# Kernel optimization log

Hardware: AMD Instinct MI355X
Metric: run time of the kernel (lower is better)

The kernel has to match this reference:

```python
import jax, jax.numpy as jnp
import numpy as np

EPS_BN = 1e-5


def _square_distance(a, b):
    # a: [B,N,3], b: [B,S,3] -> [B,N,S]
    return (jnp.sum(a * a, -1)[:, :, None]
            - 2.0 * jnp.einsum('bnc,bsc->bns', a, b)
            + jnp.sum(b * b, -1)[:, None, :])


def _bn_relu(x, gamma, beta):
    # x: [B,C,N]; training-mode batch norm over (B,N) per channel
    mean = jnp.mean(x, axis=(0, 2), keepdims=True)
    var = jnp.var(x, axis=(0, 2), keepdims=True)
    y = (x - mean) * jax.lax.rsqrt(var + EPS_BN)
    y = y * gamma[None, :, None] + beta[None, :, None]
    return jax.nn.relu(y)


def setup_inputs() -> dict:
    key = jax.random.key(0)
    ks = jax.random.split(key, 8)
    B, N, S, D1, D2 = 16, 4096, 1024, 128, 256
    Cin, C0, C1 = D1 + D2, 256, 128
    inp = {
        'xyz1': jax.random.normal(ks[0], (B, 3, N), jnp.float32),
        'xyz2': jax.random.normal(ks[1], (B, 3, S), jnp.float32),
        'points1': jax.random.normal(ks[2], (B, D1, N), jnp.float32),
        'points2': jax.random.normal(ks[3], (B, D2, S), jnp.float32),
        # pointwise Conv1d weights (kernel size 1) as [out,in]
        'w0': jax.random.normal(ks[4], (C0, Cin), jnp.float32) * (1.0 / np.sqrt(Cin)),
        'b0': jnp.zeros((C0,), jnp.float32),
        'g0': jnp.ones((C0,), jnp.float32),
        'be0': jnp.zeros((C0,), jnp.float32),
        'w1': jax.random.normal(ks[5], (C1, C0), jnp.float32) * (1.0 / np.sqrt(C0)),
        'b1': jnp.zeros((C1,), jnp.float32),
        'g1': jnp.ones((C1,), jnp.float32),
        'be1': jnp.zeros((C1,), jnp.float32),
    }
    return inp


def reference(xyz1, xyz2, points1, points2, w0, b0, g0, be0, w1, b1, g1, be1):
    # permute to [B,N,3] / [B,S,3] / [B,S,D2]
    x1 = jnp.transpose(xyz1, (0, 2, 1))
    x2 = jnp.transpose(xyz2, (0, 2, 1))
    p2 = jnp.transpose(points2, (0, 2, 1))
    B, N, _ = x1.shape

    dists = _square_distance(x1, x2)            # [B,N,S]
    # NOTE: faithful to the source: idx comes from the sort, but the
    # weight distances are the FIRST 3 columns of the UNsorted dists
    # (the repo assigns sorted values to `dicts`, not `dists`).
    idx = jnp.argsort(dists, axis=-1)[:, :, :3]  # [B,N,3]
    d3 = jnp.maximum(dists[:, :, :3], 1e-10)     # [B,N,3]
    weight = 1.0 / d3
    weight = weight / jnp.sum(weight, axis=-1, keepdims=True)

    gathered = jax.vmap(lambda p, i: p[i])(p2, idx)          # [B,N,3,D2]
    interpolated = jnp.sum(gathered * weight[..., None], axis=2)  # [B,N,D2]

    p1 = jnp.transpose(points1, (0, 2, 1))       # [B,N,D1]
    new_points = jnp.concatenate([p1, interpolated], axis=-1)  # [B,N,Cin]
    new_points = jnp.transpose(new_points, (0, 2, 1))           # [B,Cin,N]

    h = jnp.einsum('oc,bcn->bon', w0, new_points) + b0[None, :, None]
    h = _bn_relu(h, g0, be0)
    h = jnp.einsum('oc,bcn->bon', w1, h) + b1[None, :, None]
    h = _bn_relu(h, g1, be1)
    return h
```

## Files before the change

### kernel.cpp

```cpp
#include <hip/hip_runtime.h>
#include <cstdint>
#include <cstddef>

#define BB   16
#define NN   4096
#define SS   1024
#define D1   128
#define D2   256
#define CIN  384
#define C0   256
#define C1   128
#define MM   (BB*NN)
#define NBLK (MM/128)

typedef __attribute__((ext_vector_type(8))) short short8;
typedef __attribute__((ext_vector_type(4))) float f32x4;

__device__ __forceinline__ float b2f(unsigned short h) {
    union { unsigned int u; float f; } x; x.u = ((unsigned int)h) << 16; return x.f;
}
__device__ __forceinline__ unsigned short f2b(float f) {
    union { float f; unsigned int u; } x; x.f = f;
    unsigned int r = x.u + 0x7FFFu + ((x.u >> 16) & 1u);
    return (unsigned short)(r >> 16);
}

#define GLD16(g, l) __builtin_amdgcn_global_load_lds( \
    (const __attribute__((address_space(1))) void*)(g), \
    (__attribute__((address_space(3))) void*)(l), 16, 0, 0)

__device__ __forceinline__ void knn_body3(const float* __restrict__ xyz1,
                                          const float* __restrict__ xyz2,
                                          int* __restrict__ idxb, float* __restrict__ wtb,
                                          int rb, int t, char* smem)
{
    double* mrg = (double*)smem;
    const int b    = rb >> 6;
    const int lane = t & 63;
    const int n    = (rb & 63) * 64 + lane;
    const int wu   = __builtin_amdgcn_readfirstlane(t >> 6);

    const float* qx = xyz2 + ((size_t)b * 3 + 0) * SS + wu * 256;
    const float* qy = xyz2 + ((size_t)b * 3 + 1) * SS + wu * 256;
    const float* qz = xyz2 + ((size_t)b * 3 + 2) * SS + wu * 256;

    const float px = xyz1[((size_t)b * 3 + 0) * NN + n];
    const float py = xyz1[((size_t)b * 3 + 1) * NN + n];
    const float pz = xyz1[((size_t)b * 3 + 2) * NN + n];

    const double INITK = __hiloint2double(0x7F7FFFFF, 0);
    double A0 = INITK, A1 = INITK, A2 = INITK;
    double B0 = INITK, B1 = INITK, B2 = INITK;
    const int sb = wu * 256;

#pragma unroll 4
    for (int s = 0; s < 256; s += 2) {
        {
            float qxv = qx[s], qyv = qy[s], qzv = qz[s];
            float dx = px - qxv, dy = py - qyv, dz = pz - qzv;
            float d = dx*dx + dy*dy + dz*dz;
            double k = __hiloint2double(__float_as_int(d), sb + s);
            double t0 = fmin(k, A0), h0 = fmax(k, A0);
            double t1 = fmin(h0, A1), h1 = fmax(h0, A1);
            A2 = fmin(h1, A2); A0 = t0; A1 = t1;
        }
        {
            float qxv = qx[s+1], qyv = qy[s+1], qzv = qz[s+1];
            float dx = px - qxv, dy = py - qyv, dz = pz - qzv;
            float d = dx*dx + dy*dy + dz*dz;
            double k = __hiloint2double(__float_as_int(d), sb + s + 1);
            double t0 = fmin(k, B0), h0 = fmax(k, B0);
            double t1 = fmin(h0, B1), h1 = fmax(h0, B1);
            B2 = fmin(h1, B2); B0 = t0; B1 = t1;
        }
    }
    double K0, K1, K2;
    {
        double y0 = fmax(A0, B0);
        K0 = fmin(A0, B0);
        double x1 = fmin(A1, B1);
        K1 = fmin(y0, x1);
        double z  = fmax(y0, x1);
        double x2 = fmin(A2, B2);
        K2 = fmin(z, x2);
    }
    if (wu > 0) {
        mrg[(wu * 64 + lane) * 3 + 0] = K0;
        mrg[(wu * 64 + lane) * 3 + 1] = K1;
        mrg[(wu * 64 + lane) * 3 + 2] = K2;
    }
    __syncthreads();
    if (wu == 0) {
#pragma unroll
        for (int q = 1; q < 4; ++q) {
            double C0d = mrg[(q * 64 + lane) * 3 + 0];
            double C1d = mrg[(q * 64 + lane) * 3 + 1];
            double C2d = mrg[(q * 64 + lane) * 3 + 2];
            double y0 = fmax(K0, C0d);
            K0 = fmin(K0, C0d);
            double x1 = fmin(K1, C1d);
            double nK1 = fmin(y0, x1);
            double z  = fmax(y0, x1);
            double x2 = fmin(K2, C2d);
            K2 = fmin(z, x2);
            K1 = nK1;
        }
        int j0 = __double2loint(K0), j1 = __double2loint(K1), j2 = __double2loint(K2);
        float dd0, dd1, dd2;
        { float dx=px-qx[0], dy=py-qy[0], dz=pz-qz[0]; dd0 = fmaxf(dx*dx+dy*dy+dz*dz, 1e-10f); }
        { float dx=px-qx[1], dy=py-qy[1], dz=pz-qz[1]; dd1 = fmaxf(dx*dx+dy*dy+dz*dz, 1e-10f); }
        { float dx=px-qx[2], dy=py-qy[2], dz=pz-qz[2]; dd2 = fmaxf(dx*dx+dy*dy+dz*dz, 1e-10f); }
        float r0 = 1.f/dd0, r1 = 1.f/dd1, r2 = 1.f/dd2;
        float inv = 1.f / (r0 + r1 + r2);
        size_t base = ((size_t)b * NN + n) * 3;
        idxb[base+0] = j0; idxb[base+1] = j1; idxb[base+2] = j2;
        wtb[base+0] = r0*inv; wtb[base+1] = r1*inv; wtb[base+2] = r2*inv;
    }
}

__device__ __forceinline__ void transpose_body(const float* __restrict__ src,
                                               unsigned short* __restrict__ dst,
                                               int C, int Np, int dstStride,
                                               int b, int cblk, int nblk, int t, char* smem)
{
    float (*tile)[65] = (float(*)[65])smem;
    const int c0 = cblk * 64, n0 = nblk * 64;
    const int j = t & 63, i4 = t >> 6;
#pragma unroll
    for (int p = 0; p < 64; p += 4) {
        int ci = p + i4;
        tile[ci][j] = src[((size_t)b * C + c0 + ci) * Np + n0 + j];
    }
    __syncthreads();
#pragma unroll
    for (int p = 0; p < 64; p += 4) {
        int ni = p + i4;
        dst[((size_t)b * Np + n0 + ni) * dstStride + c0 + j] = f2b(tile[j][ni]);
    }
}

__global__ __launch_bounds__(256) void mega_front_k(
    const float* __restrict__ xyz1, const float* __restrict__ xyz2,
    const float* __restrict__ points1, const float* __restrict__ points2,
    const float* __restrict__ w0, const float* __restrict__ w1,
    unsigned short* __restrict__ P1T, unsigned short* __restrict__ P2T,
    unsigned short* __restrict__ w0b, unsigned short* __restrict__ w1b,
    int* __restrict__ idxb, float* __restrict__ wtb)
{
    __shared__ __align__(16) char smem[16640];
    const unsigned bid = blockIdx.x;
    const int g = bid / 70, r = bid % 70;
    const int t = threadIdx.x;

    if (r < 16) {
        knn_body3(xyz1, xyz2, idxb, wtb, g * 16 + r, t, smem);
    } else if (r < 48) {
        int rb = g * 32 + (r - 16);
        transpose_body(points1, P1T, D1, NN, D1,
                       rb >> 7, (rb >> 6) & 1, rb & 63, t, smem);
    } else if (r < 64) {
        int rb = g * 16 + (r - 48);
        transpose_body(points2, P2T, D2, SS, D2,
                       rb >> 6, (rb >> 4) & 3, rb & 15, t, smem);
    } else {
        int rb = g * 6 + (r - 64);
        int i = rb * 256 + t;
        if (i < C0 * CIN) w0b[i] = f2b(w0[i]);
        if (i < C1 * C0)  w1b[i] = f2b(w1[i]);
    }
}

__launch_bounds__(512, 1)
__global__ void gemm1_k(const unsigned short* __restrict__ P1T,
                        const unsigned short* __restrict__ P2T,
                        const int* __restrict__ idxb, const float* __restrict__ wtb,
                        const unsigned short* __restrict__ w0b,
                        unsigned short* __restrict__ h1, float* __restrict__ part1)
{
    __shared__ unsigned short Als[128 * 64];
    __shared__ unsigned short Bls[256 * 64];
    __shared__ float lsum[2][256];
    __shared__ float lsq[2][256];

    const int t = threadIdx.x;
    const int wv = t >> 6, l = t & 63, g = l >> 4, lc = l & 15;
    const int wm = wv >> 2, wn = wv & 3;
    const int m0 = blockIdx.x * 128;
    const int b  = blockIdx.x >> 5;
    const int sub = t & 7;

    const int grow = t >> 2;
    const size_t gb = ((size_t)(m0 + grow)) * 3;
    const int gi0 = idxb[gb], gi1 = idxb[gb+1], gi2 = idxb[gb+2];
    const float gw0 = wtb[gb], gw1 = wtb[gb+1], gw2 = wtb[gb+2];
    const char* gp0 = (const char*)(P2T + ((size_t)b * SS + gi0) * D2) + (t & 3) * 32;
    const char* gp1 = (const char*)(P2T + ((size_t)b * SS + gi1) * D2) + (t & 3) * 32;
    const char* gp2 = (const char*)(P2T + ((size_t)b * SS + gi2) * D2) + (t & 3) * 32;
    char* gdst = (char*)Als + grow * 128;
    const int gsw = (grow & 7) << 4;

    f32x4 acc[4][4];
#pragma unroll
    for (int i = 0; i < 4; ++i)
#pragma unroll
        for (int j = 0; j < 4; ++j) acc[i][j] = (f32x4){0.f, 0.f, 0.f, 0.f};

    for (int ks = 0; ks < 6; ++ks) {
        const int k0 = ks * 64;
        __syncthreads();
        if (ks < 2) {
#pragma unroll
            for (int q = 0; q < 2; ++q) {
                int row = q * 64 + (t >> 3);
                int bco = (sub * 16) ^ ((row & 7) << 4);
                const char* src = (const char*)P1T + (((size_t)(m0 + row)) * D1 + k0) * 2 + bco;
                char* dst = (char*)Als + (q * 512 + wv * 64) * 16;
                GLD16(src, dst);
            }
        } else {
            const int cgB = (ks - 2) * 128;
#pragma unroll
            for (int h = 0; h < 2; ++h) {
                union { uint4 v; unsigned short s[8]; } a0, a1, a2, ov;
                a0.v = *(const uint4*)(gp0 + cgB + h * 16);
                a1.v = *(const uint4*)(gp1 + cgB + h * 16);
                a2.v = *(const uint4*)(gp2 + cgB + h * 16);
#pragma unroll
                for (int i = 0; i < 8; ++i)
                    ov.s[i] = f2b(gw0 * b2f(a0.s[i]) + gw1 * b2f(a1.s[i]) + gw2 * b2f(a2.s[i]));
                *(uint4*)(gdst + (((t & 3) * 32 + h * 16) ^ gsw)) = ov.v;
            }
        }
#pragma unroll
        for (int q = 0; q < 4; ++q) {
            int o = q * 64 + (t >> 3);
            int bco = (sub * 16) ^ ((o & 7) << 4);
            const char* src = (const char*)w0b + (((size_t)o) * CIN + k0) * 2 + bco;
            char* dst = (char*)Bls + (q * 512 + wv * 64) * 16;
            GLD16(src, dst);
        }
        __syncthreads();
#pragma unroll
        for (int kk = 0; kk < 2; ++kk) {
            short8 af[4], bfr[4];
#pragma unroll
            for (int fm = 0; fm < 4; ++fm) {
                int row = wm * 64 + fm * 16 + lc;
                int bcol = kk * 64 + g * 16;
                af[fm] = *(const short8*)((const char*)Als + row * 128 + (bcol ^ ((row & 7) << 4)));
            }
#pragma unroll
            for (int fn = 0; fn < 4; ++fn) {
                int o = wn * 64 + fn * 16 + lc;
                int bcol = kk * 64 + g * 16;
                bfr[fn] = *(const short8*)((const char*)Bls + o * 128 + (bcol ^ ((o & 7) << 4)));
            }
#pragma unroll
            for (int fm = 0; fm < 4; ++fm)
#pragma unroll
                for (int fn = 0; fn < 4; ++fn)
                    acc[fm][fn] = __builtin_amdgcn_mfma_f32_16x16x32_bf16(af[fm], bfr[fn], acc[fm][fn], 0, 0, 0);
        }
    }

    float s1[4] = {0,0,0,0}, s2v[4] = {0,0,0,0};
#pragma unroll
    for (int fm = 0; fm < 4; ++fm)
#pragma unroll
        for (int fn = 0; fn < 4; ++fn) {
            int row = m0 + wm * 64 + fm * 16 + g * 4;
            int col = wn * 64 + fn * 16 + lc;
#pragma unroll
            for (int j = 0; j < 4; ++j) {
                float v = acc[fm][fn][j];
                h1[((size_t)(row + j)) * C0 + col] = f2b(v);
                s1[fn] += v; s2v[fn] += v * v;
            }
        }
#pragma unroll
    for (int fn = 0; fn < 4; ++fn) {
        s1[fn] += __shfl_xor(s1[fn], 16); s1[fn] += __shfl_xor(s1[fn], 32);
        s2v[fn] += __shfl_xor(s2v[fn], 16); s2v[fn] += __shfl_xor(s2v[fn], 32);
    }
    if (l < 16) {
#pragma unroll
        for (int fn = 0; fn < 4; ++fn) {
            lsum[wm][wn * 64 + fn * 16 + l] = s1[fn];
            lsq[wm][wn * 64 + fn * 16 + l] = s2v[fn];
        }
    }
    __syncthreads();
    if (t < 256) {
        part1[(size_t)t * NBLK + blockIdx.x]        = lsum[0][t] + lsum[1][t];
        part1[(size_t)(C0 + t) * NBLK + blockIdx.x] = lsq[0][t] + lsq[1][t];
    }
}

__global__ void stats_k(const float* __restrict__ part, int nblk, int C,
                        const float* __restrict__ gam, const float* __restrict__ bet,
                        float* __restrict__ sc, float* __restrict__ sh)
{
    const int w = threadIdx.x >> 6, l = threadIdx.x & 63;
    const int o = blockIdx.x * 4 + w;
    if (o >= C) return;
    float s = 0.f, q = 0.f;
    for (int i = l; i < nblk; i += 64) {
        s += part[(size_t)o * nblk + i];
        q += part[(size_t)(C + o) * nblk + i];
    }
#pragma unroll
    for (int r = 32; r; r >>= 1) { s += __shfl_xor(s, r); q += __shfl_xor(q, r); }
    if (l == 0) {
        const float inv = 1.0f / (float)MM;
        float mean = s * inv;
        float var = q * inv - mean * mean;
        float scale = gam[o] * rsqrtf(var + 1e-5f);
        sc[o] = scale;
        sh[o] = bet[o] - mean * scale;
    }
}

__launch_bounds__(256, 1)
__global__ void gemm2_k(const unsigned short* __restrict__ h1, const unsigned short* __restrict__ w1b,
                        const float* __restrict__ sc1, const float* __restrict__ sh1,
                        unsigned short* __restrict__ h2, float* __restrict__ part2)
{
    __shared__ unsigned short Als[128 * 64];
    __shared__ unsigned short Bls[128 * 64];
    __shared__ float scl[256], shl[256];
    __shared__ float lsum[2][128];
    __shared__ float lsq[2][128];

    const int t = threadIdx.x;
    const int wv = t >> 6, l = t & 63, g = l >> 4, lc = l & 15;
    const int wm = wv >> 1, wn = wv & 1;
    const int m0 = blockIdx.x * 128;
    const int sub = t & 7;

    scl[t] = sc1[t]; shl[t] = sh1[t];

    f32x4 acc[4][4];
#pragma unroll
    for (int i = 0; i < 4; ++i)
#pragma unroll
        for (int j = 0; j < 4; ++j) acc[i][j] = (f32x4){0.f, 0.f, 0.f, 0.f};

    for (int ks = 0; ks < 4; ++ks) {
        const int k0 = ks * 64;
        __syncthreads();
        uint4 r[4];
#pragma unroll
        for (int q = 0; q < 4; ++q) {
            int row = q * 32 + (t >> 3);
            r[q] = *(const uint4*)((const char*)h1 + (((size_t)(m0 + row)) * C0 + k0) * 2 + sub * 16);
        }
#pragma unroll
        for (int q = 0; q < 4; ++q) {
            int row = q * 32 + (t >> 3);
            union { uint4 v; unsigned short s[8]; } u, ov;
            u.v = r[q];
#pragma unroll
            for (int i = 0; i < 8; ++i) {
                int k = k0 + sub * 8 + i;
                float f = b2f(u.s[i]);
                ov.s[i] = f2b(fmaxf(0.0f, fmaf(scl[k], f, shl[k])));
            }
            *(uint4*)((char*)Als + row * 128 + ((sub * 16) ^ ((row & 7) << 4))) = ov.v;
        }
#pragma unroll
        for (int q = 0; q < 4; ++q) {
            int o = q * 32 + (t >> 3);
            int bco = (sub * 16) ^ ((o & 7) << 4);
            const char* src = (const char*)w1b + (((size_t)o) * C0 + k0) * 2 + bco;
            char* dst = (char*)Bls + (q * 256 + wv * 64) * 16;
            GLD16(src, dst);
        }
        __syncthreads();
#pragma unroll
        for (int kk = 0; kk < 2; ++kk) {
            short8 af[4], bfr[4];
#pragma unroll
            for (int fm = 0; fm < 4; ++fm) {
                int row = wm * 64 + fm * 16 + lc;
                int bcol = kk * 64 + g * 16;
                af[fm] = *(const short8*)((const char*)Als + row * 128 + (bcol ^ ((row & 7) << 4)));
            }
#pragma unroll
            for (int fn = 0; fn < 4; ++fn) {
                int o = wn * 64 + fn * 16 + lc;
                int bcol = kk * 64 + g * 16;
                bfr[fn] = *(const short8*)((const char*)Bls + o * 128 + (bcol ^ ((o & 7) << 4)));
            }
#pragma unroll
            for (int fm = 0; fm < 4; ++fm)
#pragma unroll
                for (int fn = 0; fn < 4; ++fn)
                    acc[fm][fn] = __builtin_amdgcn_mfma_f32_16x16x32_bf16(af[fm], bfr[fn], acc[fm][fn], 0, 0, 0);
        }
    }

    float s1[4] = {0,0,0,0}, s2v[4] = {0,0,0,0};
#pragma unroll
    for (int fm = 0; fm < 4; ++fm)
#pragma unroll
        for (int fn = 0; fn < 4; ++fn) {
            int row = m0 + wm * 64 + fm * 16 + g * 4;
            int col = wn * 64 + fn * 16 + lc;
#pragma unroll
            for (int j = 0; j < 4; ++j) {
                float v = acc[fm][fn][j];
                h2[((size_t)(row + j)) * C1 + col] = f2b(v);
                s1[fn] += v; s2v[fn] += v * v;
            }
        }
#pragma unroll
    for (int fn = 0; fn < 4; ++fn) {
        s1[fn] += __shfl_xor(s1[fn], 16); s1[fn] += __shfl_xor(s1[fn], 32);
        s2v[fn] += __shfl_xor(s2v[fn], 16); s2v[fn] += __shfl_xor(s2v[fn], 32);
    }
    if (l < 16) {
#pragma unroll
        for (int fn = 0; fn < 4; ++fn) {
            lsum[wm][wn * 64 + fn * 16 + l] = s1[fn];
            lsq[wm][wn * 64 + fn * 16 + l] = s2v[fn];
        }
    }
    __syncthreads();
    if (t < 128) {
        part2[(size_t)t * NBLK + blockIdx.x]        = lsum[0][t] + lsum[1][t];
        part2[(size_t)(C1 + t) * NBLK + blockIdx.x] = lsq[0][t] + lsq[1][t];
    }
}

__global__ void finalize_k(const unsigned short* __restrict__ h2,
                           const float* __restrict__ sc, const float* __restrict__ sh,
                           float* __restrict__ out)
{
    __shared__ float tile[64][65];
    const int b = blockIdx.z, o0 = blockIdx.y * 64, n0 = blockIdx.x * 64;
    const int t = threadIdx.x, j = t & 63, i4 = t >> 6;
    const float scv = sc[o0 + j], shv = sh[o0 + j];
#pragma unroll
    for (int p = 0; p < 64; p += 4) {
        int ni = p + i4;
        float f = b2f(h2[((size_t)b * NN + n0 + ni) * C1 + o0 + j]);
        tile[ni][j] = fmaxf(0.0f, fmaf(scv, f, shv));
    }
    __syncthreads();
#pragma unroll
    for (int p = 0; p < 64; p += 4) {
        int oi = p + i4;
        out[((size_t)(b * C1 + o0 + oi)) * NN + n0 + j] = tile[j][oi];
    }
}

extern "C" void kernel_launch(void* const* d_in, const int* in_sizes, int n_in,
                              void* d_out, int out_size, void* d_ws, size_t ws_size,
                              hipStream_t stream)
{
    const float* xyz1    = (const float*)d_in[0];
    const float* xyz2    = (const float*)d_in[1];
    const float* points1 = (const float*)d_in[2];
    const float* points2 = (const float*)d_in[3];
    const float* w0      = (const float*)d_in[4];
    const float* g0      = (const float*)d_in[6];
    const float* be0     = (const float*)d_in[7];
    const float* w1      = (const float*)d_in[8];
    const float* g1      = (const float*)d_in[10];
    const float* be1     = (const float*)d_in[11];
    float* out = (float*)d_out;
    char* ws = (char*)d_ws;

    unsigned short* P1T = (unsigned short*)(ws + 0);
    unsigned short* h1  = (unsigned short*)(ws + 16777216);
    unsigned short* P2T = (unsigned short*)(ws + 50331648);
    unsigned short* h2  = (unsigned short*)(ws + 58720256);
    int*   idxb  = (int*)  (ws + 75497472);
    float* wtb   = (float*)(ws + 76283904);
    unsigned short* w0b = (unsigned short*)(ws + 77070336);
    unsigned short* w1b = (unsigned short*)(ws + 77266944);
    float* part1 = (float*)(ws + 77332480);
    float* part2 = (float*)(ws + 78381056);
    float* sc1   = (float*)(ws + 78905344);
    float* sh1   = (float*)(ws + 78906368);
    float* sc2   = (float*)(ws + 78907392);
    float* sh2   = (float*)(ws + 78908416);

    mega_front_k<<<70 * 64, 256, 0, stream>>>(xyz1, xyz2, points1, points2, w0, w1,
                                              P1T, P2T, w0b, w1b, idxb, wtb);
    gemm1_k<<<MM/128, 512, 0, stream>>>(P1T, P2T, idxb, wtb, w0b, h1, part1);
    stats_k<<<C0/4, 256, 0, stream>>>(part1, NBLK, C0, g0, be0, sc1, sh1);
    gemm2_k<<<MM/128, 256, 0, stream>>>(h1, w1b, sc1, sh1, h2, part2);
    stats_k<<<C1/4, 256, 0, stream>>>(part2, NBLK, C1, g1, be1, sc2, sh2);
    finalize_k<<<dim3(NN/64, C1/64, BB), 256, 0, stream>>>(h2, sc2, sh2, out);
}
```

Before: 117.3 us.

## Split KNN candidates across 8 lanes with LDS-staged xyz2 and shuffle merge

Restructures the 3-NN search so each block handles 32 query points, with 8 lanes per point each scanning a 128-candidate chunk. Candidate coordinates are first staged into LDS as padded float4 rows, and the per-lane top-3 lists are merged with xor shuffles instead of an LDS merge plus a single-wave tail. This removes repeated global loads of xyz2 and the idle waves during the merge, at the cost of twice as many knn blocks, each with a staging pass and a barrier.

```diff
diff --git a/kernel.cpp b/kernel.cpp
--- a/kernel.cpp
+++ b/kernel.cpp
@@ -29,20 +29,24 @@
     (const __attribute__((address_space(1))) void*)(g), \
     (__attribute__((address_space(3))) void*)(l), 16, 0, 0)
 
-__device__ __forceinline__ void knn_body3(const float* __restrict__ xyz1,
+__device__ __forceinline__ void knn_body5(const float* __restrict__ xyz1,
                                           const float* __restrict__ xyz2,
                                           int* __restrict__ idxb, float* __restrict__ wtb,
                                           int rb, int t, char* smem)
 {
-    double* mrg = (double*)smem;
-    const int b    = rb >> 6;
-    const int lane = t & 63;
-    const int n    = (rb & 63) * 64 + lane;
-    const int wu   = __builtin_amdgcn_readfirstlane(t >> 6);
-
-    const float* qx = xyz2 + ((size_t)b * 3 + 0) * SS + wu * 256;
-    const float* qy = xyz2 + ((size_t)b * 3 + 1) * SS + wu * 256;
-    const float* qz = xyz2 + ((size_t)b * 3 + 2) * SS + wu * 256;
+    float4* cnd = (float4*)smem;
+    const int b    = rb >> 7;
+    const int bx   = rb & 127;
+    const int chunk = t & 7;
+    const int n    = bx * 32 + (t >> 3);
+
+    for (int i = t; i < SS; i += 256) {
+        float qx = xyz2[((size_t)b * 3 + 0) * SS + i];
+        float qy = xyz2[((size_t)b * 3 + 1) * SS + i];
+        float qz = xyz2[((size_t)b * 3 + 2) * SS + i];
+        cnd[(i >> 7) * 129 + (i & 127)] = make_float4(qx, qy, qz, 0.f);
+    }
+    __syncthreads();
 
     const float px = xyz1[((size_t)b * 3 + 0) * NN + n];
     const float py = xyz1[((size_t)b * 3 + 1) * NN + n];
@@ -51,29 +55,31 @@
     const double INITK = __hiloint2double(0x7F7FFFFF, 0);
     double A0 = INITK, A1 = INITK, A2 = INITK;
     double B0 = INITK, B1 = INITK, B2 = INITK;
-    const int sb = wu * 256;
+    const float4* cc = cnd + chunk * 129;
+    const int sbase = chunk * 128;
 
 #pragma unroll 4
-    for (int s = 0; s < 256; s += 2) {
+    for (int c = 0; c < 128; c += 2) {
         {
-            float qxv = qx[s], qyv = qy[s], qzv = qz[s];
-            float dx = px - qxv, dy = py - qyv, dz = pz - qzv;
+            float4 q = cc[c];
+            float dx = px - q.x, dy = py - q.y, dz = pz - q.z;
             float d = dx*dx + dy*dy + dz*dz;
-            double k = __hiloint2double(__float_as_int(d), sb + s);
+            double k = __hiloint2double(__float_as_int(d), sbase + c);
             double t0 = fmin(k, A0), h0 = fmax(k, A0);
             double t1 = fmin(h0, A1), h1 = fmax(h0, A1);
             A2 = fmin(h1, A2); A0 = t0; A1 = t1;
         }
         {
-            float qxv = qx[s+1], qyv = qy[s+1], qzv = qz[s+1];
-            float dx = px - qxv, dy = py - qyv, dz = pz - qzv;
+            float4 q = cc[c + 1];
+            float dx = px - q.x, dy = py - q.y, dz = pz - q.z;
             float d = dx*dx + dy*dy + dz*dz;
-            double k = __hiloint2double(__float_as_int(d), sb + s + 1);
+            double k = __hiloint2double(__float_as_int(d), sbase + c + 1);
             double t0 = fmin(k, B0), h0 = fmax(k, B0);
             double t1 = fmin(h0, B1), h1 = fmax(h0, B1);
             B2 = fmin(h1, B2); B0 = t0; B1 = t1;
         }
     }
+
     double K0, K1, K2;
     {
         double y0 = fmax(A0, B0);
@@ -81,35 +87,29 @@
         double x1 = fmin(A1, B1);
         K1 = fmin(y0, x1);
         double z  = fmax(y0, x1);
-        double x2 = fmin(A2, B2);
-        K2 = fmin(z, x2);
-    }
-    if (wu > 0) {
-        mrg[(wu * 64 + lane) * 3 + 0] = K0;
-        mrg[(wu * 64 + lane) * 3 + 1] = K1;
-        mrg[(wu * 64 + lane) * 3 + 2] = K2;
-    }
-    __syncthreads();
-    if (wu == 0) {
-#pragma unroll
-        for (int q = 1; q < 4; ++q) {
-            double C0d = mrg[(q * 64 + lane) * 3 + 0];
-            double C1d = mrg[(q * 64 + lane) * 3 + 1];
-            double C2d = mrg[(q * 64 + lane) * 3 + 2];
-            double y0 = fmax(K0, C0d);
-            K0 = fmin(K0, C0d);
-            double x1 = fmin(K1, C1d);
-            double nK1 = fmin(y0, x1);
-            double z  = fmax(y0, x1);
-            double x2 = fmin(K2, C2d);
-            K2 = fmin(z, x2);
-            K1 = nK1;
-        }
+        K2 = fmin(z, fmin(A2, B2));
+    }
+#pragma unroll
+    for (int r = 1; r <= 4; r <<= 1) {
+        double C0d = __shfl_xor(K0, r);
+        double C1d = __shfl_xor(K1, r);
+        double C2d = __shfl_xor(K2, r);
+        double y0 = fmax(K0, C0d);
+        K0 = fmin(K0, C0d);
+        double x1 = fmin(K1, C1d);
+        double nK1 = fmin(y0, x1);
+        double z  = fmax(y0, x1);
+        K2 = fmin(z, fmin(K2, C2d));
+        K1 = nK1;
+    }
+
+    if (chunk == 0) {
         int j0 = __double2loint(K0), j1 = __double2loint(K1), j2 = __double2loint(K2);
+        float4 q0 = cnd[0], q1 = cnd[1], q2 = cnd[2];
         float dd0, dd1, dd2;
-        { float dx=px-qx[0], dy=py-qy[0], dz=pz-qz[0]; dd0 = fmaxf(dx*dx+dy*dy+dz*dz, 1e-10f); }
-        { float dx=px-qx[1], dy=py-qy[1], dz=pz-qz[1]; dd1 = fmaxf(dx*dx+dy*dy+dz*dz, 1e-10f); }
-        { float dx=px-qx[2], dy=py-qy[2], dz=pz-qz[2]; dd2 = fmaxf(dx*dx+dy*dy+dz*dz, 1e-10f); }
+        { float dx=px-q0.x, dy=py-q0.y, dz=pz-q0.z; dd0 = fmaxf(dx*dx+dy*dy+dz*dz, 1e-10f); }
+        { float dx=px-q1.x, dy=py-q1.y, dz=pz-q1.z; dd1 = fmaxf(dx*dx+dy*dy+dz*dz, 1e-10f); }
+        { float dx=px-q2.x, dy=py-q2.y, dz=pz-q2.z; dd2 = fmaxf(dx*dx+dy*dy+dz*dz, 1e-10f); }
         float r0 = 1.f/dd0, r1 = 1.f/dd1, r2 = 1.f/dd2;
         float inv = 1.f / (r0 + r1 + r2);
         size_t base = ((size_t)b * NN + n) * 3;
@@ -149,21 +149,21 @@
 {
     __shared__ __align__(16) char smem[16640];
     const unsigned bid = blockIdx.x;
-    const int g = bid / 70, r = bid % 70;
+    const int g = bid / 86, r = bid % 86;
     const int t = threadIdx.x;
 
-    if (r < 16) {
-        knn_body3(xyz1, xyz2, idxb, wtb, g * 16 + r, t, smem);
-    } else if (r < 48) {
-        int rb = g * 32 + (r - 16);
+    if (r < 32) {
+        knn_body5(xyz1, xyz2, idxb, wtb, g * 32 + r, t, smem);
+    } else if (r < 64) {
+        int rb = g * 32 + (r - 32);
         transpose_body(points1, P1T, D1, NN, D1,
                        rb >> 7, (rb >> 6) & 1, rb & 63, t, smem);
-    } else if (r < 64) {
-        int rb = g * 16 + (r - 48);
+    } else if (r < 80) {
+        int rb = g * 16 + (r - 64);
         transpose_body(points2, P2T, D2, SS, D2,
                        rb >> 6, (rb >> 4) & 3, rb & 15, t, smem);
     } else {
-        int rb = g * 6 + (r - 64);
+        int rb = g * 6 + (r - 80);
         int i = rb * 256 + t;
         if (i < C0 * CIN) w0b[i] = f2b(w0[i]);
         if (i < C1 * C0)  w1b[i] = f2b(w1[i]);
@@ -486,7 +486,7 @@
     float* sc2   = (float*)(ws + 78907392);
     float* sh2   = (float*)(ws + 78908416);
 
-    mega_front_k<<<70 * 64, 256, 0, stream>>>(xyz1, xyz2, points1, points2, w0, w1,
+    mega_front_k<<<86 * 64, 256, 0, stream>>>(xyz1, xyz2, points1, points2, w0, w1,
                                               P1T, P2T, w0b, w1b, idxb, wtb);
     gemm1_k<<<MM/128, 512, 0, stream>>>(P1T, P2T, idxb, wtb, w0b, h1, part1);
     stats_k<<<C0/4, 256, 0, stream>>>(part1, NBLK, C0, g0, be0, sc1, sh1);
```

New measurement: 113.9 us. 1.03x faster.
